# Kernel tuning notes

Measured on AMD Instinct MI355X. Metric: run time of the kernel, lower is better.

The kernel has to match this reference:

```python
import jax, jax.numpy as jnp
import numpy as np
from jax import lax

COMMITMENT_COST = 0.25

def setup_inputs() -> dict:
    key = jax.random.key(0)
    k1, k2, k3, k4 = jax.random.split(key, 4)
    B, C, H, W, K = 32, 128, 32, 32, 8192
    return {
        "x": jax.random.normal(k1, (B, C, H, W), dtype=jnp.float32),
        "W_lin": jax.random.normal(k2, (C, C), dtype=jnp.float32) * (1.0 / np.sqrt(C)),
        "b_lin": jax.random.normal(k3, (C,), dtype=jnp.float32) * 0.01,
        "emb": jax.random.normal(k4, (K, C), dtype=jnp.float32),
    }

def reference(x, W_lin, b_lin, emb):
    B, C, H, W = x.shape
    K = emb.shape[0]
    # BCHW -> BHWC, then linear projection
    inp = jnp.transpose(x, (0, 2, 3, 1))          # [B,H,W,C]
    inp = inp @ W_lin.T + b_lin                   # nn.Linear
    flat = inp.reshape(-1, C)                     # [N,C], N=B*H*W
    # squared L2 distances to codebook: ||z||^2 + ||e||^2 - 2 z.e
    d = (jnp.sum(flat**2, axis=1, keepdims=True)
         + jnp.sum(emb**2, axis=1)
         - 2.0 * flat @ emb.T)                    # [N,K]
    idx = jnp.argmin(d, axis=1)                   # [N]
    quantized = emb[idx].reshape(inp.shape)       # gather == onehot @ emb
    e_latent = jnp.mean((lax.stop_gradient(quantized) - inp) ** 2)
    q_latent = jnp.mean((quantized - lax.stop_gradient(inp)) ** 2)
    loss = q_latent + COMMITMENT_COST * e_latent
    # straight-through estimator
    quantized_st = inp + lax.stop_gradient(quantized - inp)
    # perplexity from code usage histogram (== mean of one-hot encodings)
    counts = jnp.zeros((K,), dtype=flat.dtype).at[idx].add(1.0)
    avg_probs = counts / flat.shape[0]
    perplexity = jnp.exp(-jnp.sum(avg_probs * jnp.log(avg_probs + 1e-10)))
    out = jnp.transpose(quantized_st, (0, 3, 1, 2))  # back to BCHW
    return (loss, out, perplexity, idx[:, None])
```

## Files before the change

kernel.cpp:

```cpp
#include <hip/hip_runtime.h>
#include <hip/hip_bf16.h>
#include <float.h>

#define NPIX   32768
#define CDIM   128
#define KCB    8192
#define EPS_STOP 0.30f
#define TAUF   0.012f
#define RCAP   8192
#define RCAPA  2048

typedef _Float16 f16x8 __attribute__((ext_vector_type(8)));
typedef float    f32x16 __attribute__((ext_vector_type(16)));

#define WS_EMBFH   0
#define WS_E2      2359296
#define WS_ZWS     2392064
#define WS_CAND    19169280
#define WS_IDX     20217856
#define WS_RLISTA  20348928
#define WS_RLISTB  20381696
#define WS_SCAND   20512768
#define WS_SCANI   21037056
#define WS_COUNTS  21299200
#define WS_LOSS    21331968
#define WS_RCNTA   21331972
#define WS_RCNTB   21331976
#define WS_ZERO_OFF 21299200
#define WS_ZERO_LEN 32780

#define OUT_OFF_OUT  1
#define OUT_OFF_PERP 4194305
#define OUT_OFF_IDX  4194306

__device__ __forceinline__ float min3f(float a, float b, float c) {
    return fminf(fminf(a, b), c);
}

__device__ __forceinline__ void ins6(float f, float v[6]) {
    float a = fmaxf(v[0], f); v[0] = fminf(v[0], f);
    float b = fmaxf(v[1], a); v[1] = fminf(v[1], a);
    a = fmaxf(v[2], b); v[2] = fminf(v[2], b);
    b = fmaxf(v[3], a); v[3] = fminf(v[3], a);
    a = fmaxf(v[4], b); v[4] = fminf(v[4], b);
    v[5] = fminf(v[5], a);
}

__global__ __launch_bounds__(256) void k_e2(const float* __restrict__ emb, float* __restrict__ e2) {
    int t = threadIdx.x;
    int wv = t >> 6, l = t & 63;
    int k = blockIdx.x * 4 + wv;
    const float2 v = *(const float2*)&emb[(size_t)k * 128 + l * 2];
    float s = v.x * v.x + v.y * v.y;
    #pragma unroll
    for (int o = 32; o; o >>= 1) s += __shfl_down(s, o, 64);
    if (l == 0) e2[k] = s;
}

__global__ __launch_bounds__(256) void k_prep(const float* __restrict__ emb, const float* __restrict__ e2,
                                              _Float16* __restrict__ embFh) {
    int tid = blockIdx.x * 256 + threadIdx.x;
    int m = tid / 18, r = tid % 18;
    int s = r >> 1, h = r & 1;
    f16x8 hv;
    #pragma unroll
    for (int j = 0; j < 8; ++j) hv[j] = (_Float16)0.0f;
    if (s < 8) {
        int c0 = s * 16 + h * 8;
        const float4 a = *(const float4*)&emb[(size_t)m * 128 + c0];
        const float4 b = *(const float4*)&emb[(size_t)m * 128 + c0 + 4];
        float vals[8] = {a.x, a.y, a.z, a.w, b.x, b.y, b.z, b.w};
        #pragma unroll
        for (int j = 0; j < 8; ++j) hv[j] = (_Float16)(-2.0f * vals[j]);
    } else if (h == 0) {
        float v = e2[m] + 512.0f;
        _Float16 eh = (_Float16)v;
        hv[0] = eh;
        hv[1] = (_Float16)(v - (float)eh);
    }
    size_t base = (((size_t)(m >> 5) * 9 + s) * 64 + (m & 31) + h * 32) * 8;
    *(f16x8*)&embFh[base] = hv;
}

__global__ __launch_bounds__(512, 4) void k_main(
    const float* __restrict__ x, const float* __restrict__ Wl, const float* __restrict__ bl,
    const _Float16* __restrict__ embFh,
    float* __restrict__ zws, float4* __restrict__ cand)
{
    __shared__ __align__(16) float As[64 * 132];
    __shared__ __align__(16) float Xs[64 * 66];
    __shared__ float z2p[64 * 8];

    const int t  = threadIdx.x;
    const int n0 = blockIdx.x * 64;
    const int b  = n0 >> 10;
    const int hw0 = n0 & 1023;

    {
        const int p = t & 63, ig = t >> 6;
        float accz[16];
        const float4* bl4 = (const float4*)(bl + ig * 16);
        #pragma unroll
        for (int q = 0; q < 4; ++q) {
            float4 v = bl4[q];
            accz[4*q+0] = v.x; accz[4*q+1] = v.y; accz[4*q+2] = v.z; accz[4*q+3] = v.w;
        }
        for (int hf = 0; hf < 2; ++hf) {
            __syncthreads();
            for (int r = 0; r < 8; ++r) {
                int lin = r * 512 + t;
                int cc = lin >> 6, pp = lin & 63;
                Xs[cc * 66 + pp] = x[(size_t)(b * 128 + hf * 64 + cc) * 1024 + hw0 + pp];
            }
            __syncthreads();
            for (int cc4 = 0; cc4 < 16; ++cc4) {
                float xv0 = Xs[(cc4*4+0) * 66 + p];
                float xv1 = Xs[(cc4*4+1) * 66 + p];
                float xv2 = Xs[(cc4*4+2) * 66 + p];
                float xv3 = Xs[(cc4*4+3) * 66 + p];
                #pragma unroll
                for (int ii = 0; ii < 16; ++ii) {
                    const float4 w4 = *(const float4*)&Wl[(size_t)(ig*16+ii) * 128 + hf*64 + cc4*4];
                    float a = accz[ii];
                    a = fmaf(w4.x, xv0, a);
                    a = fmaf(w4.y, xv1, a);
                    a = fmaf(w4.z, xv2, a);
                    a = fmaf(w4.w, xv3, a);
                    accz[ii] = a;
                }
            }
        }
        float ssq = 0.f;
        float4* ao = (float4*)&As[p * 132 + ig * 16];
        float4* zo = (float4*)(zws + (size_t)(n0 + p) * 128 + ig * 16);
        #pragma unroll
        for (int q = 0; q < 4; ++q) {
            float4 v = make_float4(accz[4*q+0], accz[4*q+1], accz[4*q+2], accz[4*q+3]);
            ao[q] = v;
            zo[q] = v;
            ssq = fmaf(v.x, v.x, fmaf(v.y, v.y, fmaf(v.z, v.z, fmaf(v.w, v.w, ssq))));
        }
        z2p[p * 8 + ig] = ssq;
    }
    __syncthreads();

    const int l = t & 63, w = t >> 6;
    const int half = l >> 5, pcol = l & 31;
    const int px = ((w >> 2) << 5) + pcol;
    f16x8 B[9];
    #pragma unroll
    for (int s = 0; s < 8; ++s) {
        const float* zp = &As[px * 132 + s * 16 + half * 8];
        float4 v0 = *(const float4*)zp;
        float4 v1 = *(const float4*)(zp + 4);
        float vals[8] = {v0.x, v0.y, v0.z, v0.w, v1.x, v1.y, v1.z, v1.w};
        f16x8 hh;
        #pragma unroll
        for (int j2 = 0; j2 < 8; ++j2) hh[j2] = (_Float16)vals[j2];
        B[s] = hh;
    }
    {
        f16x8 b8;
        #pragma unroll
        for (int j2 = 0; j2 < 8; ++j2) b8[j2] = (_Float16)0.0f;
        if (half == 0) { b8[0] = (_Float16)1.0f; b8[1] = (_Float16)1.0f; }
        B[8] = b8;
    }

    auto tree16 = [](const f32x16& v) -> float {
        float a = min3f(v[0], v[1], v[2]);
        float bb = min3f(v[3], v[4], v[5]);
        float c = min3f(v[6], v[7], v[8]);
        float d = min3f(v[9], v[10], v[11]);
        float e = min3f(v[12], v[13], v[14]);
        float f = fminf(v[15], a);
        return min3f(min3f(bb, c, d), e, f);
    };

    float gv[6] = {3e38f, 3e38f, 3e38f, 3e38f, 3e38f, 3e38f};
    const f16x8* Ahp = (const f16x8*)embFh;

    for (int g = (w & 3); g < 256; g += 4) {
        const f16x8* P = Ahp + (size_t)g * 576 + l;
        f16x8 a[9];
        #pragma unroll
        for (int s = 0; s < 9; ++s) a[s] = P[s * 64];

        f32x16 c00 = {}, c01 = {};
        __builtin_amdgcn_s_setprio(1);
        #pragma unroll
        for (int s = 0; s < 9; ++s) {
            if (s & 1) c01 = __builtin_amdgcn_mfma_f32_32x32x16_f16(a[s], B[s], c01, 0, 0, 0);
            else       c00 = __builtin_amdgcn_mfma_f32_32x32x16_f16(a[s], B[s], c00, 0, 0, 0);
        }
        __builtin_amdgcn_s_setprio(0);

        f32x16 s0;
        #pragma unroll
        for (int r = 0; r < 16; ++r) s0[r] = c00[r] + c01[r];
        float m0 = tree16(s0);
        uint32_t id = (uint32_t)((g << 1) | half);
        ins6(__uint_as_float((__float_as_uint(m0) & 0xFFFFFE00u) | id), gv);
    }

    __syncthreads();
    float* Ms = Xs;
    const int slot = ((w & 3) << 1) | half;
    #pragma unroll
    for (int q = 0; q < 6; ++q) Ms[(px * 8 + slot) * 6 + q] = gv[q];
    __syncthreads();
    if (t < 64) {
        float v6[6] = {3e38f, 3e38f, 3e38f, 3e38f, 3e38f, 3e38f};
        #pragma unroll
        for (int s = 0; s < 48; ++s) ins6(Ms[t * 48 + s], v6);
        float z2 = 0.f;
        #pragma unroll
        for (int q = 0; q < 8; ++q) z2 += z2p[t * 8 + q];
        cand[(size_t)(n0 + t) * 2 + 0] = make_float4(v6[0], v6[1], v6[2], v6[3]);
        cand[(size_t)(n0 + t) * 2 + 1] = make_float4(v6[4], v6[5], z2, 0.f);
    }
}

__global__ __launch_bounds__(256) void k_rec(
    const float* __restrict__ zws, const float* __restrict__ emb,
    const float4* __restrict__ cand, int* __restrict__ idxws,
    float* __restrict__ out_idxf, float* __restrict__ losssum,
    int* __restrict__ rlistA, int* __restrict__ rcntA,
    int* __restrict__ rlistB, int* __restrict__ rcntB)
{
    __shared__ float lred[16];
    const int t = threadIdx.x;
    const int pl = t >> 4, j = t & 15;
    const int n = blockIdx.x * 16 + pl;

    const float4 za = *(const float4*)&zws[(size_t)n * 128 + j * 8];
    const float4 zb = *(const float4*)&zws[(size_t)n * 128 + j * 8 + 4];
    const float4 c0 = cand[(size_t)n * 2 + 0];
    const float4 c1 = cand[(size_t)n * 2 + 1];
    const float pv[6] = {c0.x, c0.y, c0.z, c0.w, c1.x, c1.y};
    const float pbase = c1.z - 512.0f;

    float d1 = 3e38f, d2 = 3e38f; int i1 = 0x7fffffff, i2 = 0x7fffffff;
    bool safe = false;
    float lastgmin = 0.f;
    for (int q = 0; q < 6; ++q) {
        uint32_t bits = __float_as_uint(pv[q]);
        float gmin = __uint_as_float(bits & 0xFFFFFE00u);
        lastgmin = gmin;
        if (gmin >= d1 - pbase + EPS_STOP) { safe = true; break; }
        const int mbase = (int)((bits >> 1) & 255u) * 32 + (int)((bits & 1u) << 2);
        #pragma unroll
        for (int c = 0; c < 16; ++c) {
            int m = mbase + (c & 3) + 8 * (c >> 2);
            const float4 ea = *(const float4*)&emb[(size_t)m * 128 + j * 8];
            const float4 eb = *(const float4*)&emb[(size_t)m * 128 + j * 8 + 4];
            float da0 = za.x - ea.x, da1 = za.y - ea.y, da2 = za.z - ea.z, da3 = za.w - ea.w;
            float db0 = zb.x - eb.x, db1 = zb.y - eb.y, db2 = zb.z - eb.z, db3 = zb.w - eb.w;
            float s = da0*da0; s = fmaf(da1, da1, s); s = fmaf(da2, da2, s); s = fmaf(da3, da3, s);
            s = fmaf(db0, db0, s); s = fmaf(db1, db1, s); s = fmaf(db2, db2, s); s = fmaf(db3, db3, s);
            s += __shfl_xor(s, 1, 16);
            s += __shfl_xor(s, 2, 16);
            s += __shfl_xor(s, 4, 16);
            s += __shfl_xor(s, 8, 16);
            if (s < d1 || (s == d1 && m < i1)) { d2 = d1; i2 = i1; d1 = s; i1 = m; }
            else if (s < d2) { d2 = s; i2 = m; }
        }
    }
    if (!safe && lastgmin >= d1 - pbase + EPS_STOP) safe = true;

    if (j == 0) {
        idxws[n] = i1;
        out_idxf[n] = (float)i1;
        if (!safe) {
            int s = atomicAdd(rcntA, 1);
            if (s < RCAPA) rlistA[s] = n;
        } else if ((d2 - d1) < TAUF) {
            int s = atomicAdd(rcntB, 1);
            if (s < RCAP) { int4 v4 = make_int4(n, i1, i2, 0); ((int4*)rlistB)[s] = v4; }
        }
        lred[pl] = d1;
    }
    __syncthreads();
    if (t == 0) {
        float ls = 0.f;
        #pragma unroll
        for (int q = 0; q < 16; ++q) ls += lred[q];
        atomicAdd(losssum, ls);
    }
}

__global__ __launch_bounds__(256) void k_scanp(
    const float* __restrict__ zws, const float* __restrict__ emb,
    const int* __restrict__ rcntA, const int* __restrict__ rlistA,
    double* __restrict__ scand, int* __restrict__ scani)
{
    int cnt = *rcntA; if (cnt > RCAPA) cnt = RCAPA;
    const int t = threadIdx.x;
    const int chunk = blockIdx.x & 31;
    const int gi = t >> 4, j = t & 15;
    __shared__ double sd[16];
    __shared__ int si[16];
    for (int e = blockIdx.x >> 5; e < cnt; e += 64) {
        const int n = rlistA[e];
        const float4 za = *(const float4*)&zws[(size_t)n * 128 + j * 8];
        const float4 zb = *(const float4*)&zws[(size_t)n * 128 + j * 8 + 4];
        double best = 1e300; int bi = 0x7fffffff;
        const int kbase = chunk * 256 + gi * 16;
        for (int c = 0; c < 16; ++c) {
            const int m = kbase + c;
            const float4 ea = *(const float4*)&emb[(size_t)m * 128 + j * 8];
            const float4 eb = *(const float4*)&emb[(size_t)m * 128 + j * 8 + 4];
            double s = 0.0, d;
            d = (double)za.x - (double)ea.x; s += d * d;
            d = (double)za.y - (double)ea.y; s += d * d;
            d = (double)za.z - (double)ea.z; s += d * d;
            d = (double)za.w - (double)ea.w; s += d * d;
            d = (double)zb.x - (double)eb.x; s += d * d;
            d = (double)zb.y - (double)eb.y; s += d * d;
            d = (double)zb.z - (double)eb.z; s += d * d;
            d = (double)zb.w - (double)eb.w; s += d * d;
            s += __shfl_xor(s, 1, 16);
            s += __shfl_xor(s, 2, 16);
            s += __shfl_xor(s, 4, 16);
            s += __shfl_xor(s, 8, 16);
            if (s < best) { best = s; bi = m; }
        }
        __syncthreads();
        if (j == 0) { sd[gi] = best; si[gi] = bi; }
        __syncthreads();
        if (t == 0) {
            double b = sd[0]; int ib = si[0];
            #pragma unroll
            for (int q = 1; q < 16; ++q)
                if (sd[q] < b || (sd[q] == b && si[q] < ib)) { b = sd[q]; ib = si[q]; }
            scand[e * 32 + chunk] = b;
            scani[e * 32 + chunk] = ib;
        }
    }
}

__global__ __launch_bounds__(64) void k_mergeA(
    const int* __restrict__ rcntA, const int* __restrict__ rlistA,
    const double* __restrict__ scand, const int* __restrict__ scani,
    int* __restrict__ idxws, float* __restrict__ out_idxf)
{
    int cnt = *rcntA; if (cnt > RCAPA) cnt = RCAPA;
    const int t = threadIdx.x;
    for (int e = blockIdx.x; e < cnt; e += gridDim.x) {
        double b = 1e300; int ib = 0x7fffffff;
        if (t < 32) { b = scand[e * 32 + t]; ib = scani[e * 32 + t]; }
        #pragma unroll
        for (int o = 16; o; o >>= 1) {
            double ob = __shfl_down(b, o, 64);
            int oi = __shfl_down(ib, o, 64);
            if (ob < b || (ob == b && oi < ib)) { b = ob; ib = oi; }
        }
        if (t == 0) { int n = rlistA[e]; idxws[n] = ib; out_idxf[n] = (float)ib; }
    }
}

__global__ __launch_bounds__(128) void k_pairB(
    const float* __restrict__ x, const float* __restrict__ Wl, const float* __restrict__ bl,
    const float* __restrict__ emb, const int* __restrict__ rcntB, const int* __restrict__ rlistB,
    int* __restrict__ idxws, float* __restrict__ out_idxf)
{
    __shared__ double xs[128];
    __shared__ double red[128];
    int cnt = *rcntB; if (cnt > RCAP) cnt = RCAP;
    const int t = threadIdx.x;
    for (int e = blockIdx.x; e < cnt; e += gridDim.x) {
        const int4 v = ((const int4*)rlistB)[e];
        const int n = v.x, c1 = v.y, c2 = v.z;
        const int b = n >> 10, hw = n & 1023;
        __syncthreads();
        xs[t] = (double)x[(size_t)(b * 128 + t) * 1024 + hw];
        __syncthreads();
        double z = (double)bl[t];
        for (int c = 0; c < 128; ++c) z = fma((double)Wl[(size_t)t * 128 + c], xs[c], z);
        double d1v, d2v;
        double da = z - (double)emb[(size_t)c1 * 128 + t];
        red[t] = da * da; __syncthreads();
        for (int o = 64; o; o >>= 1) { if (t < o) red[t] += red[t + o]; __syncthreads(); }
        d1v = red[0]; __syncthreads();
        double db = z - (double)emb[(size_t)c2 * 128 + t];
        red[t] = db * db; __syncthreads();
        for (int o = 64; o; o >>= 1) { if (t < o) red[t] += red[t + o]; __syncthreads(); }
        d2v = red[0];
        if (t == 0) {
            int win = (d2v < d1v || (d2v == d1v && c2 < c1)) ? c2 : c1;
            idxws[n] = win;
            out_idxf[n] = (float)win;
        }
        __syncthreads();
    }
}

__global__ __launch_bounds__(256) void k_out(
    const float* __restrict__ emb, const int* __restrict__ idxws,
    float* __restrict__ outp , float* __restrict__ counts)
{
    const int t = threadIdx.x;
    const int b = blockIdx.x >> 2, h0 = (blockIdx.x & 3) << 3;
    const int n = b * 1024 + h0 * 32 + t;
    const int id = idxws[n];
    atomicAdd(&counts[id], 1.0f);
    const float4* ep = (const float4*)&emb[(size_t)id * 128];
    float* ob = outp + (size_t)b * 131072 + h0 * 32 + t;
    #pragma unroll 4
    for (int c4 = 0; c4 < 32; ++c4) {
        float4 v = ep[c4];
        ob[(c4 * 4 + 0) * 1024] = v.x;
        ob[(c4 * 4 + 1) * 1024] = v.y;
        ob[(c4 * 4 + 2) * 1024] = v.z;
        ob[(c4 * 4 + 3) * 1024] = v.w;
    }
}

__global__ __launch_bounds__(256) void k_final(
    const float* __restrict__ counts, const float* __restrict__ losssum, float* __restrict__ d_out)
{
    const int t = threadIdx.x;
    float ent = 0.f;
    for (int k = t; k < KCB; k += 256) {
        float p = counts[k] * (1.0f / 32768.0f);
        ent -= p * logf(p + 1e-10f);
    }
    #pragma unroll
    for (int o = 32; o; o >>= 1) ent += __shfl_down(ent, o, 64);
    __shared__ float wred[4];
    if ((t & 63) == 0) wred[t >> 6] = ent;
    __syncthreads();
    if (t == 0) {
        float e = wred[0] + wred[1] + wred[2] + wred[3];
        d_out[0] = 1.25f * (*losssum) * (1.0f / 4194304.0f);
        d_out[OUT_OFF_PERP] = expf(e);
    }
}

extern "C" void kernel_launch(void* const* d_in, const int* in_sizes, int n_in,
                              void* d_out, int out_size, void* d_ws, size_t ws_size,
                              hipStream_t stream) {
    (void)in_sizes; (void)n_in; (void)out_size; (void)ws_size;
    const float* x   = (const float*)d_in[0];
    const float* Wl  = (const float*)d_in[1];
    const float* bl  = (const float*)d_in[2];
    const float* emb = (const float*)d_in[3];
    float* out = (float*)d_out;
    char*  ws  = (char*)d_ws;

    _Float16* embFh = (_Float16*)(ws + WS_EMBFH);
    float* e2      = (float*)(ws + WS_E2);
    float* zws     = (float*)(ws + WS_ZWS);
    float4* cand   = (float4*)(ws + WS_CAND);
    int*   idxws   = (int*)  (ws + WS_IDX);
    int*   rlistA  = (int*)  (ws + WS_RLISTA);
    int*   rlistB  = (int*)  (ws + WS_RLISTB);
    double* scand  = (double*)(ws + WS_SCAND);
    int*   scani   = (int*)  (ws + WS_SCANI);
    float* counts  = (float*)(ws + WS_COUNTS);
    float* losssum = (float*)(ws + WS_LOSS);
    int*   rcntA   = (int*)  (ws + WS_RCNTA);
    int*   rcntB   = (int*)  (ws + WS_RCNTB);

    hipMemsetAsync(ws + WS_ZERO_OFF, 0, WS_ZERO_LEN, stream);

    k_e2<<<KCB / 4, 256, 0, stream>>>(emb, e2);
    k_prep<<<576, 256, 0, stream>>>(emb, e2, embFh);
    k_main<<<NPIX / 64, 512, 0, stream>>>(x, Wl, bl, embFh, zws, cand);
    k_rec<<<NPIX / 16, 256, 0, stream>>>(zws, emb, cand, idxws, out + OUT_OFF_IDX,
                                         losssum, rlistA, rcntA, rlistB, rcntB);
    k_scanp<<<2048, 256, 0, stream>>>(zws, emb, rcntA, rlistA, scand, scani);
    k_mergeA<<<32, 64, 0, stream>>>(rcntA, rlistA, scand, scani, idxws, out + OUT_OFF_IDX);
    k_pairB<<<256, 128, 0, stream>>>(x, Wl, bl, emb, rcntB, rlistB, idxws, out + OUT_OFF_IDX);
    k_out<<<128, 256, 0, stream>>>(emb, idxws, out + OUT_OFF_OUT, counts);
    k_final<<<1, 256, 0, stream>>>(counts, losssum, out);
}
```

Baseline: 318.1 us.

## Software-pipeline codebook MFMA loop with double-buffered accumulators and prefetch

Restructures the codebook scan in k_main into a software pipeline. The MFMA burst for one tile now overlaps the min-reduction tail of the previous tile, and the next tile's fragments are prefetched. It also uses four independent accumulators to shorten MFMA dependency chains and relaxes launch bounds from 4 to 2 waves per SIMD to free registers. The cost is higher register pressure (two sets of four 16-float accumulators) and possibly lower occupancy.

```diff
diff --git a/kernel.cpp b/kernel.cpp
--- a/kernel.cpp
+++ b/kernel.cpp
@@ -46,6 +46,10 @@
     v[5] = fminf(v[5], a);
 }
 
+__device__ __forceinline__ float packmin(float m, uint32_t id) {
+    return __uint_as_float((__float_as_uint(m) & 0xFFFFFE00u) | id);
+}
+
 __global__ __launch_bounds__(256) void k_e2(const float* __restrict__ emb, float* __restrict__ e2) {
     int t = threadIdx.x;
     int wv = t >> 6, l = t & 63;
@@ -82,7 +86,7 @@
     *(f16x8*)&embFh[base] = hv;
 }
 
-__global__ __launch_bounds__(512, 4) void k_main(
+__global__ __launch_bounds__(512, 2) void k_main(
     const float* __restrict__ x, const float* __restrict__ Wl, const float* __restrict__ bl,
     const _Float16* __restrict__ embFh,
     float* __restrict__ zws, float4* __restrict__ cand)
@@ -173,35 +177,56 @@
         float c = min3f(v[6], v[7], v[8]);
         float d = min3f(v[9], v[10], v[11]);
         float e = min3f(v[12], v[13], v[14]);
-        float f = fminf(v[15], a);
-        return min3f(min3f(bb, c, d), e, f);
+        float f = min3f(a, bb, c);
+        float g = min3f(d, e, v[15]);
+        return fminf(f, g);
     };
 
     float gv[6] = {3e38f, 3e38f, 3e38f, 3e38f, 3e38f, 3e38f};
     const f16x8* Ahp = (const f16x8*)embFh;
-
-    for (int g = (w & 3); g < 256; g += 4) {
-        const f16x8* P = Ahp + (size_t)g * 576 + l;
-        f16x8 a[9];
-        #pragma unroll
-        for (int s = 0; s < 9; ++s) a[s] = P[s * 64];
-
-        f32x16 c00 = {}, c01 = {};
-        __builtin_amdgcn_s_setprio(1);
-        #pragma unroll
-        for (int s = 0; s < 9; ++s) {
-            if (s & 1) c01 = __builtin_amdgcn_mfma_f32_32x32x16_f16(a[s], B[s], c01, 0, 0, 0);
-            else       c00 = __builtin_amdgcn_mfma_f32_32x32x16_f16(a[s], B[s], c00, 0, 0, 0);
-        }
-        __builtin_amdgcn_s_setprio(0);
-
-        f32x16 s0;
-        #pragma unroll
-        for (int r = 0; r < 16; ++r) s0[r] = c00[r] + c01[r];
-        float m0 = tree16(s0);
-        uint32_t id = (uint32_t)((g << 1) | half);
-        ins6(__uint_as_float((__float_as_uint(m0) & 0xFFFFFE00u) | id), gv);
-    }
+    const int gbase = w & 3;
+    f16x8 aC[9];
+    f32x16 P[4], Q[4];
+
+    #define LOADA(i_) { \
+        const f16x8* Pp = Ahp + (size_t)(gbase + 4 * (i_)) * 576 + l; \
+        _Pragma("unroll") \
+        for (int s = 0; s < 9; ++s) aC[s] = Pp[s * 64]; \
+    }
+    #define BURST(C_) { \
+        _Pragma("unroll") \
+        for (int c = 0; c < 4; ++c) C_[c] = (f32x16){}; \
+        _Pragma("unroll") \
+        for (int s = 0; s < 9; ++s) \
+            C_[s & 3] = __builtin_amdgcn_mfma_f32_32x32x16_f16(aC[s], B[s], C_[s & 3], 0, 0, 0); \
+    }
+    #define TAIL(C_, i_) { \
+        f32x16 s0; \
+        _Pragma("unroll") \
+        for (int r = 0; r < 16; ++r) s0[r] = (C_[0][r] + C_[1][r]) + (C_[2][r] + C_[3][r]); \
+        float m0 = tree16(s0); \
+        uint32_t id = (uint32_t)(((gbase + 4 * (i_)) << 1) | half); \
+        ins6(packmin(m0, id), gv); \
+    }
+
+    LOADA(0);
+    BURST(P);
+    LOADA(1);
+    for (int i = 0; i < 31; ++i) {
+        BURST(Q);
+        LOADA(2 * i + 2);
+        TAIL(P, 2 * i);
+        BURST(P);
+        LOADA(2 * i + 3);
+        TAIL(Q, 2 * i + 1);
+    }
+    BURST(Q);
+    TAIL(P, 62);
+    TAIL(Q, 63);
+
+    #undef LOADA
+    #undef BURST
+    #undef TAIL
 
     __syncthreads();
     float* Ms = Xs;
```

After: 328.4 us. 3.2% more time.
